# Kernel optimization log

Hardware: AMD Instinct MI355X
Metric: run time of the kernel (lower is better)

Reference implementation:

```python
import jax, jax.numpy as jnp
import numpy as np

DIM = 1024
N_HIDDEN = 64
NUM_HEADS = 16
B, S = 4, 1024
# original torch code: scale = sqrt(n_hidden // num_heads) = sqrt(64 // 16) = 2.0
SCALE = float(np.sqrt(N_HIDDEN // NUM_HEADS))


def setup_inputs() -> dict:
    key = jax.random.key(0)
    ks = jax.random.split(key, 10)
    lim = 1.0 / np.sqrt(DIM)          # nn.Linear default init range
    lim_o = 1.0 / np.sqrt(N_HIDDEN * NUM_HEADS)
    u = lambda k, shape, l: jax.random.uniform(k, shape, jnp.float32, -l, l)
    x = jax.random.normal(ks[0], (B, S, DIM), jnp.float32)
    attn_mask = jax.random.randint(ks[1], (B, S, S), 0, 2).astype(jnp.int32)
    # stacked per-head projection weights: [H, dim, n_hidden]
    Wq = u(ks[2], (NUM_HEADS, DIM, N_HIDDEN), lim)
    bq = u(ks[3], (NUM_HEADS, N_HIDDEN), lim)
    Wk = u(ks[4], (NUM_HEADS, DIM, N_HIDDEN), lim)
    bk = u(ks[5], (NUM_HEADS, N_HIDDEN), lim)
    Wv = u(ks[6], (NUM_HEADS, DIM, N_HIDDEN), lim)
    bv = u(ks[7], (NUM_HEADS, N_HIDDEN), lim)
    Wo = u(ks[8], (NUM_HEADS * N_HIDDEN, DIM), lim_o)
    bo = u(ks[9], (DIM,), lim_o)
    return {"x": x, "attn_mask": attn_mask, "Wq": Wq, "bq": bq,
            "Wk": Wk, "bk": bk, "Wv": Wv, "bv": bv, "Wo": Wo, "bo": bo}


def reference(x, attn_mask, Wq, bq, Wk, bk, Wv, bv, Wo, bo):
    # batched QKV across all heads (replaces the per-head Python loop)
    Q = jnp.einsum('bsd,hde->bhse', x, Wq) + bq[None, :, None, :]
    K = jnp.einsum('bsd,hde->bhse', x, Wk) + bk[None, :, None, :]
    V = jnp.einsum('bsd,hde->bhse', x, Wv) + bv[None, :, None, :]
    scores = jnp.einsum('bhse,bhte->bhst', Q, K) / SCALE
    alpha = jax.nn.softmax(scores, axis=-1)
    # faithful to original: zero out masked entries AFTER softmax, no renorm
    alpha = jnp.where(attn_mask[:, None, :, :] == 0, 0.0, alpha)  # [B,H,S,S]
    out = jnp.einsum('bhst,bhte->bhse', alpha, V)                 # [B,H,S,E]
    # torch.cat over heads on last dim == reshape to [B,S,H*E] in head order
    concat = out.transpose(0, 2, 1, 3).reshape(B, S, NUM_HEADS * N_HIDDEN)
    attn_output = concat @ Wo + bo                                # [B,S,dim]
    return attn_output, alpha
```

## Files before the change

### kernel.cpp

```cpp
#include <hip/hip_runtime.h>
#include <stdint.h>

#define S_LEN 1024
#define DIM   1024
#define NHID  64
#define NHEAD 16
#define NB    4

typedef __bf16 bf16x8 __attribute__((ext_vector_type(8)));
typedef float  f32x4  __attribute__((ext_vector_type(4)));
typedef unsigned short u16;

__device__ __forceinline__ u16 f2b(float f) {
  unsigned u = __float_as_uint(f);
  u += 0x7FFFu + ((u >> 16) & 1u);
  return (u16)(u >> 16);
}

__device__ __forceinline__ f32x4 mfma16(bf16x8 a, bf16x8 b, f32x4 c) {
  return __builtin_amdgcn_mfma_f32_16x16x32_bf16(a, b, c, 0, 0, 0);
}

__global__ __launch_bounds__(256) void k_cvt_x(const float* __restrict__ x,
                                               u16* __restrict__ xb) {
  int i = blockIdx.x * 256 + threadIdx.x;
  float4 v = ((const float4*)x)[i];
  ushort4 o;
  o.x = f2b(v.x); o.y = f2b(v.y); o.z = f2b(v.z); o.w = f2b(v.w);
  ((ushort4*)xb)[i] = o;
}

__global__ __launch_bounds__(256) void k_maskbits(const int* __restrict__ mask,
                                                  uint32_t* __restrict__ bits) {
  int w = blockIdx.x * 256 + threadIdx.x;
  const int4* mp = (const int4*)mask + (size_t)w * 8;
  uint32_t v = 0;
#pragma unroll
  for (int i = 0; i < 8; ++i) {
    int4 m = mp[i];
    v |= (m.x != 0 ? 1u : 0u) << (i * 4 + 0);
    v |= (m.y != 0 ? 1u : 0u) << (i * 4 + 1);
    v |= (m.z != 0 ? 1u : 0u) << (i * 4 + 2);
    v |= (m.w != 0 ? 1u : 0u) << (i * 4 + 3);
  }
  bits[w] = v;
}

__global__ __launch_bounds__(256) void k_transpose(const float* __restrict__ in,
                                                   u16* __restrict__ out,
                                                   int R, int C) {
  const float* ip = in + (size_t)blockIdx.x * R * C;
  u16* op = out + (size_t)blockIdx.x * R * C;
  __shared__ float tile[32][65];
  int r0 = blockIdx.y * 32, c0 = blockIdx.z * 64;
  int t = threadIdx.x;
  {
    int col = t & 63, rr = t >> 6;
#pragma unroll
    for (int p = 0; p < 8; ++p) {
      int r = p * 4 + rr;
      tile[r][col] = ip[(size_t)(r0 + r) * C + c0 + col];
    }
  }
  __syncthreads();
  {
    int d = t & 31, er = t >> 5;
#pragma unroll
    for (int p = 0; p < 8; ++p) {
      int e = p * 8 + er;
      op[(size_t)(c0 + e) * R + r0 + d] = f2b(tile[d][e]);
    }
  }
}

__global__ __launch_bounds__(256) void k_qkv(const u16* __restrict__ xb,
                                             const u16* __restrict__ Wtb,
                                             const float* __restrict__ bq,
                                             const float* __restrict__ bk,
                                             const float* __restrict__ bv,
                                             u16* __restrict__ Qb,
                                             u16* __restrict__ Kb,
                                             u16* __restrict__ Vtb) {
  __shared__ __align__(16) char lds[32768];
  int t = threadIdx.x, w = t >> 6, lane = t & 63;
  int l15 = lane & 15, l4 = lane >> 4;
  int m0 = blockIdx.x * 128, n0 = blockIdx.y * 128, sel = blockIdx.z;
  const u16* Wh = Wtb + (size_t)sel * (NHEAD * NHID * DIM);
  int wr = w >> 1, wc = w & 1;

  f32x4 acc[4][4];
  const f32x4 fz = {0.f, 0.f, 0.f, 0.f};
#pragma unroll
  for (int i = 0; i < 4; ++i)
#pragma unroll
    for (int j = 0; j < 4; ++j) acc[i][j] = fz;

  for (int kk = 0; kk < 16; ++kk) {
    int k0 = kk * 64;
#pragma unroll
    for (int c = 0; c < 4; ++c) {
      int idx = c * 256 + t, r = idx >> 3, cb = idx & 7;
      int4 v = *(const int4*)(xb + (size_t)(m0 + r) * DIM + k0 + cb * 8);
      *(int4*)(lds + r * 128 + ((cb * 16) ^ ((r & 7) << 4))) = v;
    }
#pragma unroll
    for (int c = 0; c < 4; ++c) {
      int idx = c * 256 + t, r = idx >> 3, cb = idx & 7;
      int4 v = *(const int4*)(Wh + (size_t)(n0 + r) * DIM + k0 + cb * 8);
      *(int4*)(lds + 16384 + r * 128 + ((cb * 16) ^ ((r & 7) << 4))) = v;
    }
    __syncthreads();
    bf16x8 a[4][2], bb[4][2];
#pragma unroll
    for (int mf = 0; mf < 4; ++mf)
#pragma unroll
      for (int kc = 0; kc < 2; ++kc) {
        int row = wr * 64 + mf * 16 + l15;
        int kb = kc * 64 + l4 * 16;
        a[mf][kc] = *(const bf16x8*)(lds + row * 128 + (kb ^ ((row & 7) << 4)));
      }
#pragma unroll
    for (int nf = 0; nf < 4; ++nf)
#pragma unroll
      for (int kc = 0; kc < 2; ++kc) {
        int row = wc * 64 + nf * 16 + l15;
        int kb = kc * 64 + l4 * 16;
        bb[nf][kc] = *(const bf16x8*)(lds + 16384 + row * 128 + (kb ^ ((row & 7) << 4)));
      }
#pragma unroll
    for (int kc = 0; kc < 2; ++kc)
#pragma unroll
      for (int mf = 0; mf < 4; ++mf)
#pragma unroll
        for (int nf = 0; nf < 4; ++nf)
          acc[mf][nf] = mfma16(a[mf][kc], bb[nf][kc], acc[mf][nf]);
    __syncthreads();
  }

  const float* bias = (sel == 0) ? bq : (sel == 1) ? bk : bv;
  float postScale = (sel == 0) ? 0.5f : 1.0f;
#pragma unroll
  for (int nf = 0; nf < 4; ++nf) {
    int n = n0 + wc * 64 + nf * 16 + l15;
    int h = n >> 6, e = n & 63;
    float bv_ = bias[n];
#pragma unroll
    for (int mf = 0; mf < 4; ++mf) {
      int mrow0 = m0 + wr * 64 + mf * 16 + l4 * 4;
      int b_ = mrow0 >> 10, s0 = mrow0 & 1023;
      if (sel == 2) {
        ushort4 pk;
        pk.x = f2b(acc[mf][nf][0] + bv_);
        pk.y = f2b(acc[mf][nf][1] + bv_);
        pk.z = f2b(acc[mf][nf][2] + bv_);
        pk.w = f2b(acc[mf][nf][3] + bv_);
        *(ushort4*)(Vtb + ((size_t)(b_ * NHEAD + h) * NHID + e) * S_LEN + s0) = pk;
      } else {
        u16* dst = (sel == 0) ? Qb : Kb;
#pragma unroll
        for (int j = 0; j < 4; ++j)
          dst[((size_t)(b_ * NHEAD + h) * S_LEN + s0 + j) * NHID + e] =
              f2b((acc[mf][nf][j] + bv_) * postScale);
      }
    }
  }
}

__global__ __launch_bounds__(256) void k_attn(const u16* __restrict__ Qb,
                                              const u16* __restrict__ Kb,
                                              const u16* __restrict__ Vtb,
                                              const uint32_t* __restrict__ mbitsG,
                                              float* __restrict__ alphaOut,
                                              u16* __restrict__ Ob) {
  __shared__ __align__(16) char smem[33024];
  float* redS = (float*)(smem + 32768);
  int t = threadIdx.x, w = t >> 6, lane = t & 63;
  int l15 = lane & 15, l4 = lane >> 4;
  int q0 = blockIdx.x * 16;
  int bh = blockIdx.y, b = bh >> 4, hh = bh & 15;
  const u16* Qh = Qb + (size_t)bh * S_LEN * NHID;
  const u16* Kh = Kb + (size_t)bh * S_LEN * NHID;
  const u16* Vh = Vtb + (size_t)bh * NHID * S_LEN;
  int kbase = w * 256;

  const uint32_t* mrow = mbitsG + ((size_t)b * S_LEN + q0 + l15) * 32 + w * 8;
  uint4 mw0 = *(const uint4*)(mrow);
  uint4 mw1 = *(const uint4*)(mrow + 4);

  bf16x8 aq[2];
#pragma unroll
  for (int ec = 0; ec < 2; ++ec)
    aq[ec] = *(const bf16x8*)(Qh + (size_t)(q0 + l15) * NHID + ec * 32 + l4 * 8);

  const f32x4 fz = {0.f, 0.f, 0.f, 0.f};

  float s0 = 0.f, s1 = 0.f, s2 = 0.f, s3 = 0.f;
#pragma unroll
  for (int kf = 0; kf < 16; ++kf) {
    int key = kbase + kf * 16 + l15;
    bf16x8 kb0 = *(const bf16x8*)(Kh + (size_t)key * NHID + l4 * 8);
    bf16x8 kb1 = *(const bf16x8*)(Kh + (size_t)key * NHID + 32 + l4 * 8);
    f32x4 sct = fz;
    sct = mfma16(kb0, aq[0], sct);
    sct = mfma16(kb1, aq[1], sct);
    float e0 = __expf(sct[0]);
    float e1 = __expf(sct[1]);
    float e2 = __expf(sct[2]);
    float e3 = __expf(sct[3]);
    s0 += e0; s1 += e1; s2 += e2; s3 += e3;
    uint32_t mword;
    switch (kf >> 1) {
      case 0: mword = mw0.x; break;
      case 1: mword = mw0.y; break;
      case 2: mword = mw0.z; break;
      case 3: mword = mw0.w; break;
      case 4: mword = mw1.x; break;
      case 5: mword = mw1.y; break;
      case 6: mword = mw1.z; break;
      default: mword = mw1.w; break;
    }
    int bbase = ((kf & 1) << 4) + l4 * 4;
    uint32_t am01 = (((mword >> (bbase + 0)) & 1u) ? 0x0000FFFFu : 0u) |
                    (((mword >> (bbase + 1)) & 1u) ? 0xFFFF0000u : 0u);
    uint32_t am23 = (((mword >> (bbase + 2)) & 1u) ? 0x0000FFFFu : 0u) |
                    (((mword >> (bbase + 3)) & 1u) ? 0xFFFF0000u : 0u);
    uint2 pk;
    pk.x = ((uint32_t)f2b(e0) | ((uint32_t)f2b(e1) << 16)) & am01;
    pk.y = ((uint32_t)f2b(e2) | ((uint32_t)f2b(e3) << 16)) & am23;
    *(uint2*)(smem + l15 * 2048 +
              (((kbase + kf * 16 + l4 * 4) * 2) ^ ((l15 & 7) << 4))) = pk;
  }
  float ls = (s0 + s1) + (s2 + s3);
  ls += __shfl_xor(ls, 16);
  ls += __shfl_xor(ls, 32);
  if (lane < 16) redS[w * 16 + l15] = ls;
  __syncthreads();

  float* abW = alphaOut + (size_t)bh * S_LEN * S_LEN;
  f32x4 o[4];
#pragma unroll
  for (int ef = 0; ef < 4; ++ef) o[ef] = fz;

  auto rw = [&](int rr) {
    int r = w * 4 + rr;
    float invr = 1.f / (redS[r] + redS[16 + r] + redS[32 + r] + redS[48 + r]);
    float* dst = abW + (size_t)(q0 + r) * S_LEN;
#pragma unroll
    for (int seg = 0; seg < 4; ++seg) {
      int raw = seg * 512 + lane * 8;
      int boff = raw ^ ((r & 7) << 4);
      uint2 pk = *(const uint2*)(smem + r * 2048 + boff);
      f32x4 av;
      av[0] = __uint_as_float(pk.x << 16) * invr;
      av[1] = __uint_as_float(pk.x & 0xFFFF0000u) * invr;
      av[2] = __uint_as_float(pk.y << 16) * invr;
      av[3] = __uint_as_float(pk.y & 0xFFFF0000u) * invr;
      __builtin_nontemporal_store(av, (f32x4*)(dst + (raw >> 1)));
    }
  };
  auto pvc = [&](int c) {
#pragma unroll
    for (int kc2 = 0; kc2 < 2; ++kc2) {
      bf16x8 pa = *(const bf16x8*)(smem + l15 * 2048 +
          ((((kbase + c * 64 + kc2 * 32) * 2) + l4 * 16) ^ ((l15 & 7) << 4)));
#pragma unroll
      for (int ef = 0; ef < 4; ++ef) {
        int e = ef * 16 + l15;
        bf16x8 vb = *(const bf16x8*)(Vh + (size_t)e * S_LEN + kbase + c * 64 +
                                     kc2 * 32 + l4 * 8);
        o[ef] = mfma16(pa, vb, o[ef]);
      }
    }
  };

  rw(0); pvc(0);
  rw(1); pvc(1);
  rw(2); pvc(2);
  rw(3); pvc(3);

  __syncthreads();
  float* redO = (float*)smem;
#pragma unroll
  for (int ef = 0; ef < 4; ++ef)
#pragma unroll
    for (int j = 0; j < 4; ++j)
      redO[w * 1024 + (l4 * 4 + j) * 64 + ef * 16 + l15] = o[ef][j];
  __syncthreads();
  {
    int e = t & 63, r4 = t >> 6;
#pragma unroll
    for (int p = 0; p < 4; ++p) {
      int r = p * 4 + r4;
      float invr = 1.f / (redS[r] + redS[16 + r] + redS[32 + r] + redS[48 + r]);
      float s4 = redO[r * 64 + e] + redO[1024 + r * 64 + e] +
                 redO[2048 + r * 64 + e] + redO[3072 + r * 64 + e];
      Ob[(size_t)(b * S_LEN + q0 + r) * DIM + hh * NHID + e] = f2b(s4 * invr);
    }
  }
}

__global__ __launch_bounds__(256) void k_oproj(const u16* __restrict__ Ob,
                                               const u16* __restrict__ Wotb,
                                               const float* __restrict__ bo,
                                               float* __restrict__ out) {
  __shared__ __align__(16) char lds[32768];
  int t = threadIdx.x, w = t >> 6, lane = t & 63;
  int l15 = lane & 15, l4 = lane >> 4;
  int m0 = blockIdx.x * 128, n0 = blockIdx.y * 128;
  int wr = w >> 1, wc = w & 1;
  f32x4 acc[4][4];
  const f32x4 fz = {0.f, 0.f, 0.f, 0.f};
#pragma unroll
  for (int i = 0; i < 4; ++i)
#pragma unroll
    for (int j = 0; j < 4; ++j) acc[i][j] = fz;

  for (int kk = 0; kk < 16; ++kk) {
    int k0 = kk * 64;
#pragma unroll
    for (int c = 0; c < 4; ++c) {
      int idx = c * 256 + t, r = idx >> 3, cb = idx & 7;
      int4 v = *(const int4*)(Ob + (size_t)(m0 + r) * DIM + k0 + cb * 8);
      *(int4*)(lds + r * 128 + ((cb * 16) ^ ((r & 7) << 4))) = v;
    }
#pragma unroll
    for (int c = 0; c < 4; ++c) {
      int idx = c * 256 + t, r = idx >> 3, cb = idx & 7;
      int4 v = *(const int4*)(Wotb + (size_t)(n0 + r) * DIM + k0 + cb * 8);
      *(int4*)(lds + 16384 + r * 128 + ((cb * 16) ^ ((r & 7) << 4))) = v;
    }
    __syncthreads();
    bf16x8 a[4][2], bb[4][2];
#pragma unroll
    for (int mf = 0; mf < 4; ++mf)
#pragma unroll
      for (int kc = 0; kc < 2; ++kc) {
        int row = wr * 64 + mf * 16 + l15;
        int kb = kc * 64 + l4 * 16;
        a[mf][kc] = *(const bf16x8*)(lds + row * 128 + (kb ^ ((row & 7) << 4)));
      }
#pragma unroll
    for (int nf = 0; nf < 4; ++nf)
#pragma unroll
      for (int kc = 0; kc < 2; ++kc) {
        int row = wc * 64 + nf * 16 + l15;
        int kb = kc * 64 + l4 * 16;
        bb[nf][kc] = *(const bf16x8*)(lds + 16384 + row * 128 + (kb ^ ((row & 7) << 4)));
      }
#pragma unroll
    for (int kc = 0; kc < 2; ++kc)
#pragma unroll
      for (int mf = 0; mf < 4; ++mf)
#pragma unroll
        for (int nf = 0; nf < 4; ++nf)
          acc[mf][nf] = mfma16(a[mf][kc], bb[nf][kc], acc[mf][nf]);
    __syncthreads();
  }
#pragma unroll
  for (int nf = 0; nf < 4; ++nf) {
    int n = n0 + wc * 64 + nf * 16 + l15;
    float bv_ = bo[n];
#pragma unroll
    for (int mf = 0; mf < 4; ++mf)
#pragma unroll
      for (int j = 0; j < 4; ++j) {
        int m = m0 + wr * 64 + mf * 16 + l4 * 4 + j;
        out[(size_t)m * DIM + n] = acc[mf][nf][j] + bv_;
      }
  }
}

extern "C" void kernel_launch(void* const* d_in, const int* in_sizes, int n_in,
                              void* d_out, int out_size, void* d_ws, size_t ws_size,
                              hipStream_t stream) {
  const float* x    = (const float*)d_in[0];
  const int*   mask = (const int*)d_in[1];
  const float* Wq   = (const float*)d_in[2];
  const float* bq   = (const float*)d_in[3];
  const float* Wk   = (const float*)d_in[4];
  const float* bk   = (const float*)d_in[5];
  const float* Wv   = (const float*)d_in[6];
  const float* bv   = (const float*)d_in[7];
  const float* Wo   = (const float*)d_in[8];
  const float* bo   = (const float*)d_in[9];
  float* out = (float*)d_out;
  float* alphaOut = out + (size_t)NB * S_LEN * DIM;

  char* ws = (char*)d_ws;
  u16* xb    = (u16*)(ws);
  u16* Wtb   = (u16*)(ws + 8388608);
  u16* Wotb  = (u16*)(ws + 14680064);
  u16* Qb    = (u16*)(ws + 16777216);
  u16* Kb    = (u16*)(ws + 25165824);
  u16* Vtb   = (u16*)(ws + 33554432);
  u16* Ob    = (u16*)(ws + 41943040);
  uint32_t* mbits = (uint32_t*)(ws + 50331648);

  k_maskbits<<<512, 256, 0, stream>>>(mask, mbits);
  k_cvt_x<<<4096, 256, 0, stream>>>(x, xb);
  k_transpose<<<dim3(16, 32, 1), 256, 0, stream>>>(Wq, Wtb,           1024, 64);
  k_transpose<<<dim3(16, 32, 1), 256, 0, stream>>>(Wk, Wtb + 1048576, 1024, 64);
  k_transpose<<<dim3(16, 32, 1), 256, 0, stream>>>(Wv, Wtb + 2097152, 1024, 64);
  k_transpose<<<dim3(1, 32, 16), 256, 0, stream>>>(Wo, Wotb,          1024, 1024);
  k_qkv<<<dim3(32, 8, 3), 256, 0, stream>>>(xb, Wtb, bq, bk, bv, Qb, Kb, Vtb);
  k_attn<<<dim3(64, 64), 256, 0, stream>>>(Qb, Kb, Vtb, mbits, alphaOut, Ob);
  k_oproj<<<dim3(32, 8), 256, 0, stream>>>(Ob, Wotb, bo, out);
}
```

Before: 219.3 us.

## Split attention keys across 8 waves and use direct global-to-LDS loads in GEMMs

The attention kernel now runs 512 threads per block, so each of 8 waves handles 128 keys instead of 256, and the per-row sum and output reductions go across 8 partials. This is meant to raise occupancy and latency hiding for the memory-bound alpha writes. Separately, the QKV and output-projection GEMMs, when the builtin is available, load tiles with global_load_lds, with the XOR swizzle applied on the global side, which skips the register staging. The cost is larger cross-wave reductions, and the LDS writes depend on the builtin's lane-ordered layout matching the swizzle the readers expect.

```diff
diff --git a/kernel.cpp b/kernel.cpp
--- a/kernel.cpp
+++ b/kernel.cpp
@@ -10,6 +10,19 @@
 typedef __bf16 bf16x8 __attribute__((ext_vector_type(8)));
 typedef float  f32x4  __attribute__((ext_vector_type(4)));
 typedef unsigned short u16;
+
+#if defined(__has_builtin)
+#if __has_builtin(__builtin_amdgcn_global_load_lds)
+#define HAS_GLD 1
+#endif
+#endif
+
+#ifdef HAS_GLD
+#define GLD16(gsrc, ldst)                                                    \
+  __builtin_amdgcn_global_load_lds(                                         \
+      (const __attribute__((address_space(1))) unsigned int*)(gsrc),        \
+      (__attribute__((address_space(3))) unsigned int*)(ldst), 16, 0, 0)
+#endif
 
 __device__ __forceinline__ u16 f2b(float f) {
   unsigned u = __float_as_uint(f);
@@ -97,6 +110,22 @@
 
   for (int kk = 0; kk < 16; ++kk) {
     int k0 = kk * 64;
+#ifdef HAS_GLD
+#pragma unroll
+    for (int c = 0; c < 4; ++c) {
+      int idx = c * 256 + t, r = idx >> 3, cb = idx & 7;
+      int sc_ = cb ^ (r & 7);
+      GLD16(xb + (size_t)(m0 + r) * DIM + k0 + sc_ * 8,
+            lds + (c * 256 + w * 64) * 16);
+    }
+#pragma unroll
+    for (int c = 0; c < 4; ++c) {
+      int idx = c * 256 + t, r = idx >> 3, cb = idx & 7;
+      int sc_ = cb ^ (r & 7);
+      GLD16(Wh + (size_t)(n0 + r) * DIM + k0 + sc_ * 8,
+            lds + 16384 + (c * 256 + w * 64) * 16);
+    }
+#else
 #pragma unroll
     for (int c = 0; c < 4; ++c) {
       int idx = c * 256 + t, r = idx >> 3, cb = idx & 7;
@@ -109,6 +138,7 @@
       int4 v = *(const int4*)(Wh + (size_t)(n0 + r) * DIM + k0 + cb * 8);
       *(int4*)(lds + 16384 + r * 128 + ((cb * 16) ^ ((r & 7) << 4))) = v;
     }
+#endif
     __syncthreads();
     bf16x8 a[4][2], bb[4][2];
 #pragma unroll
@@ -166,13 +196,13 @@
   }
 }
 
-__global__ __launch_bounds__(256) void k_attn(const u16* __restrict__ Qb,
-                                              const u16* __restrict__ Kb,
-                                              const u16* __restrict__ Vtb,
-                                              const uint32_t* __restrict__ mbitsG,
-                                              float* __restrict__ alphaOut,
-                                              u16* __restrict__ Ob) {
-  __shared__ __align__(16) char smem[33024];
+__global__ __launch_bounds__(512, 8) void k_attn(const u16* __restrict__ Qb,
+                                                 const u16* __restrict__ Kb,
+                                                 const u16* __restrict__ Vtb,
+                                                 const uint32_t* __restrict__ mbitsG,
+                                                 float* __restrict__ alphaOut,
+                                                 u16* __restrict__ Ob) {
+  __shared__ __align__(16) char smem[33280];
   float* redS = (float*)(smem + 32768);
   int t = threadIdx.x, w = t >> 6, lane = t & 63;
   int l15 = lane & 15, l4 = lane >> 4;
@@ -181,11 +211,9 @@
   const u16* Qh = Qb + (size_t)bh * S_LEN * NHID;
   const u16* Kh = Kb + (size_t)bh * S_LEN * NHID;
   const u16* Vh = Vtb + (size_t)bh * NHID * S_LEN;
-  int kbase = w * 256;
-
-  const uint32_t* mrow = mbitsG + ((size_t)b * S_LEN + q0 + l15) * 32 + w * 8;
-  uint4 mw0 = *(const uint4*)(mrow);
-  uint4 mw1 = *(const uint4*)(mrow + 4);
+  int kbase = w * 128;
+
+  uint4 mw = *(const uint4*)(mbitsG + ((size_t)b * S_LEN + q0 + l15) * 32 + w * 4);
 
   bf16x8 aq[2];
 #pragma unroll
@@ -196,7 +224,7 @@
 
   float s0 = 0.f, s1 = 0.f, s2 = 0.f, s3 = 0.f;
 #pragma unroll
-  for (int kf = 0; kf < 16; ++kf) {
+  for (int kf = 0; kf < 8; ++kf) {
     int key = kbase + kf * 16 + l15;
     bf16x8 kb0 = *(const bf16x8*)(Kh + (size_t)key * NHID + l4 * 8);
     bf16x8 kb1 = *(const bf16x8*)(Kh + (size_t)key * NHID + 32 + l4 * 8);
@@ -210,14 +238,10 @@
     s0 += e0; s1 += e1; s2 += e2; s3 += e3;
     uint32_t mword;
     switch (kf >> 1) {
-      case 0: mword = mw0.x; break;
-      case 1: mword = mw0.y; break;
-      case 2: mword = mw0.z; break;
-      case 3: mword = mw0.w; break;
-      case 4: mword = mw1.x; break;
-      case 5: mword = mw1.y; break;
-      case 6: mword = mw1.z; break;
-      default: mword = mw1.w; break;
+      case 0: mword = mw.x; break;
+      case 1: mword = mw.y; break;
+      case 2: mword = mw.z; break;
+      default: mword = mw.w; break;
     }
     int bbase = ((kf & 1) << 4) + l4 * 4;
     uint32_t am01 = (((mword >> (bbase + 0)) & 1u) ? 0x0000FFFFu : 0u) |
@@ -236,14 +260,21 @@
   if (lane < 16) redS[w * 16 + l15] = ls;
   __syncthreads();
 
+  auto rowInv = [&](int r) {
+    float s = 0.f;
+#pragma unroll
+    for (int wi = 0; wi < 8; ++wi) s += redS[wi * 16 + r];
+    return 1.f / s;
+  };
+
   float* abW = alphaOut + (size_t)bh * S_LEN * S_LEN;
   f32x4 o[4];
 #pragma unroll
   for (int ef = 0; ef < 4; ++ef) o[ef] = fz;
 
   auto rw = [&](int rr) {
-    int r = w * 4 + rr;
-    float invr = 1.f / (redS[r] + redS[16 + r] + redS[32 + r] + redS[48 + r]);
+    int r = w * 2 + rr;
+    float invr = rowInv(r);
     float* dst = abW + (size_t)(q0 + r) * S_LEN;
 #pragma unroll
     for (int seg = 0; seg < 4; ++seg) {
@@ -275,8 +306,6 @@
 
   rw(0); pvc(0);
   rw(1); pvc(1);
-  rw(2); pvc(2);
-  rw(3); pvc(3);
 
   __syncthreads();
   float* redO = (float*)smem;
@@ -287,14 +316,15 @@
       redO[w * 1024 + (l4 * 4 + j) * 64 + ef * 16 + l15] = o[ef][j];
   __syncthreads();
   {
-    int e = t & 63, r4 = t >> 6;
-#pragma unroll
-    for (int p = 0; p < 4; ++p) {
-      int r = p * 4 + r4;
-      float invr = 1.f / (redS[r] + redS[16 + r] + redS[32 + r] + redS[48 + r]);
-      float s4 = redO[r * 64 + e] + redO[1024 + r * 64 + e] +
-                 redO[2048 + r * 64 + e] + redO[3072 + r * 64 + e];
-      Ob[(size_t)(b * S_LEN + q0 + r) * DIM + hh * NHID + e] = f2b(s4 * invr);
+    int e = t & 63, r8 = t >> 6;
+#pragma unroll
+    for (int p = 0; p < 2; ++p) {
+      int r = r8 * 2 + p;
+      float invr = rowInv(r);
+      float s8 = 0.f;
+#pragma unroll
+      for (int wi = 0; wi < 8; ++wi) s8 += redO[wi * 1024 + r * 64 + e];
+      Ob[(size_t)(b * S_LEN + q0 + r) * DIM + hh * NHID + e] = f2b(s8 * invr);
     }
   }
 }
@@ -317,6 +347,22 @@
 
   for (int kk = 0; kk < 16; ++kk) {
     int k0 = kk * 64;
+#ifdef HAS_GLD
+#pragma unroll
+    for (int c = 0; c < 4; ++c) {
+      int idx = c * 256 + t, r = idx >> 3, cb = idx & 7;
+      int sc_ = cb ^ (r & 7);
+      GLD16(Ob + (size_t)(m0 + r) * DIM + k0 + sc_ * 8,
+            lds + (c * 256 + w * 64) * 16);
+    }
+#pragma unroll
+    for (int c = 0; c < 4; ++c) {
+      int idx = c * 256 + t, r = idx >> 3, cb = idx & 7;
+      int sc_ = cb ^ (r & 7);
+      GLD16(Wotb + (size_t)(n0 + r) * DIM + k0 + sc_ * 8,
+            lds + 16384 + (c * 256 + w * 64) * 16);
+    }
+#else
 #pragma unroll
     for (int c = 0; c < 4; ++c) {
       int idx = c * 256 + t, r = idx >> 3, cb = idx & 7;
@@ -329,6 +375,7 @@
       int4 v = *(const int4*)(Wotb + (size_t)(n0 + r) * DIM + k0 + cb * 8);
       *(int4*)(lds + 16384 + r * 128 + ((cb * 16) ^ ((r & 7) << 4))) = v;
     }
+#endif
     __syncthreads();
     bf16x8 a[4][2], bb[4][2];
 #pragma unroll
@@ -403,6 +450,6 @@
   k_transpose<<<dim3(16, 32, 1), 256, 0, stream>>>(Wv, Wtb + 2097152, 1024, 64);
   k_transpose<<<dim3(1, 32, 16), 256, 0, stream>>>(Wo, Wotb,          1024, 1024);
   k_qkv<<<dim3(32, 8, 3), 256, 0, stream>>>(xb, Wtb, bq, bk, bv, Qb, Kb, Vtb);
-  k_attn<<<dim3(64, 64), 256, 0, stream>>>(Qb, Kb, Vtb, mbits, alphaOut, Ob);
+  k_attn<<<dim3(64, 64), 512, 0, stream>>>(Qb, Kb, Vtb, mbits, alphaOut, Ob);
   k_oproj<<<dim3(32, 8), 256, 0, stream>>>(Ob, Wotb, bo, out);
 }
```

Measured after the change: 233.4 us. 1.06x slower.
